# Kernel tuning notes

Measured on AMD Instinct MI355X. Metric: run time of the kernel, lower is better.

## Reference

```python
import jax, jax.numpy as jnp
import numpy as np

NH, NL, NP = 8, 4, 4  # n_heads, n_levels, n_points


def _layer_norm(x, g, b, eps=1e-5):
    mu = x.mean(-1, keepdims=True)
    var = ((x - mu) ** 2).mean(-1, keepdims=True)
    return (x - mu) * jax.lax.rsqrt(var + eps) * g + b


def setup_inputs() -> dict:
    key = jax.random.key(0)
    ks = jax.random.split(key, 16)
    B, C, DFF = 2, 256, 1024
    ss = np.array([[128, 128], [64, 64], [32, 32], [16, 16]], np.int32)
    lsi = np.concatenate([[0], np.cumsum(ss[:, 0] * ss[:, 1])[:-1]]).astype(np.int32)
    Lq = int((ss[:, 0] * ss[:, 1]).sum())  # 21760
    w = lambda k, shp: (jax.random.normal(k, shp, jnp.float32) * 0.02)
    return {
        "src": jax.random.normal(ks[0], (B, Lq, C), jnp.float32),
        "pos": jax.random.normal(ks[1], (B, Lq, C), jnp.float32),
        "reference_points": jax.random.uniform(ks[2], (B, Lq, NL, 2), jnp.float32),
        "spatial_shapes": jnp.asarray(ss),
        "level_start_index": jnp.asarray(lsi),
        "Wv": w(ks[3], (C, C)), "bv": jnp.zeros((C,), jnp.float32),
        "Woff": w(ks[4], (C, NH * NL * NP * 2)), "boff": jnp.zeros((NH * NL * NP * 2,), jnp.float32),
        "Wa": w(ks[5], (C, NH * NL * NP)), "ba": jnp.zeros((NH * NL * NP,), jnp.float32),
        "Wo": w(ks[6], (C, C)), "bo": jnp.zeros((C,), jnp.float32),
        "W1": w(ks[7], (C, DFF)), "b1": jnp.zeros((DFF,), jnp.float32),
        "W2": w(ks[8], (DFF, C)), "b2": jnp.zeros((C,), jnp.float32),
        "g1": jnp.ones((C,), jnp.float32), "be1": jnp.zeros((C,), jnp.float32),
        "g2": jnp.ones((C,), jnp.float32), "be2": jnp.zeros((C,), jnp.float32),
    }


def _ms_deform_attn(value, ss, lsi, loc, attn):
    # value: [B,L,NH,Dh]; loc: [B,Lq,NH,NL,NP,2] in [0,1]; attn: [B,Lq,NH,NL,NP]
    B, Lq = loc.shape[0], loc.shape[1]
    Dh = value.shape[-1]
    out = jnp.zeros((B, NH, Lq, Dh), value.dtype)
    for l in range(NL):
        H_, W_ = int(ss[l, 0]), int(ss[l, 1])
        start = int(lsi[l])
        val = value[:, start:start + H_ * W_].transpose(0, 2, 1, 3)  # [B,NH,HW,Dh]
        x = loc[:, :, :, l, :, 0] * W_ - 0.5  # grid_sample align_corners=False
        y = loc[:, :, :, l, :, 1] * H_ - 0.5  # [B,Lq,NH,NP]
        x0f, y0f = jnp.floor(x), jnp.floor(y)
        lx, ly = x - x0f, y - y0f
        x0, y0 = x0f.astype(jnp.int32), y0f.astype(jnp.int32)
        acc = jnp.zeros((B, NH, Lq, NP, Dh), value.dtype)
        for dy, dx, wgt in ((0, 0, (1 - ly) * (1 - lx)), (0, 1, (1 - ly) * lx),
                            (1, 0, ly * (1 - lx)), (1, 1, ly * lx)):
            yi, xi = y0 + dy, x0 + dx
            valid = ((yi >= 0) & (yi < H_) & (xi >= 0) & (xi < W_)).astype(value.dtype)
            idx = jnp.clip(yi, 0, H_ - 1) * W_ + jnp.clip(xi, 0, W_ - 1)  # [B,Lq,NH,NP]
            idxT = idx.transpose(0, 2, 1, 3).reshape(B, NH, Lq * NP, 1)
            v = jnp.take_along_axis(val, idxT, axis=2).reshape(B, NH, Lq, NP, Dh)
            acc = acc + v * (wgt * valid).transpose(0, 2, 1, 3)[..., None]
        out = out + (acc * attn[:, :, :, l].transpose(0, 2, 1, 3)[..., None]).sum(3)
    return out.transpose(0, 2, 1, 3).reshape(B, Lq, NH * Dh)


def reference(src, pos, reference_points, spatial_shapes, level_start_index,
              Wv, bv, Woff, boff, Wa, ba, Wo, bo, W1, b1, W2, b2, g1, be1, g2, be2):
    ss = np.asarray(spatial_shapes)
    lsi = np.asarray(level_start_index)
    B, Lq, C = src.shape
    Dh = C // NH
    q = src + pos  # with_pos_embed
    value = (src @ Wv + bv).reshape(B, Lq, NH, Dh)
    offs = (q @ Woff + boff).reshape(B, Lq, NH, NL, NP, 2)
    attn = jax.nn.softmax((q @ Wa + ba).reshape(B, Lq, NH, NL * NP), -1).reshape(B, Lq, NH, NL, NP)
    # offset normalizer is (W, H) per level
    norm = jnp.asarray(ss[:, ::-1].astype(np.float32))  # [NL,2]
    loc = reference_points[:, :, None, :, None, :] + offs / norm[None, None, None, :, None, :]
    src2 = _ms_deform_attn(value, ss, lsi, loc, attn) @ Wo + bo
    x = _layer_norm(src + src2, g1, be1)
    ff = jax.nn.relu(x @ W1 + b1) @ W2 + b2
    return _layer_norm(x + ff, g2, be2)
```

## Files before the change

### kernel.cpp

```cpp
#include <hip/hip_runtime.h>
#include <hip/hip_bf16.h>

#define B_    2
#define LQ    21760
#define NROW  (B_*LQ)
#define CDIM  256
#define DFF   1024

typedef __attribute__((ext_vector_type(8))) short bf16x8;
typedef __attribute__((ext_vector_type(4))) float f32x4;
typedef __attribute__((ext_vector_type(2))) float f32x2;

static __device__ __forceinline__ ushort f2bf(float f) {
    union { float f; unsigned u; } v; v.f = f;
    unsigned u = v.u;
    return (ushort)((u + 0x7fffu + ((u >> 16) & 1u)) >> 16);
}
static __device__ __forceinline__ float u2f(unsigned u) {
    union { unsigned u; float f; } v; v.u = u; return v.f;
}
static __device__ __forceinline__ float bf2f(ushort h) {
    return u2f(((unsigned)h) << 16);
}
static __device__ __forceinline__ unsigned char f2fp8(float v) {
    return (unsigned char)(__builtin_amdgcn_cvt_pk_fp8_f32(v, v, 0, false) & 0xff);
}
static __device__ __forceinline__ int swzc(int row, int col) {
    return (col & ~63) | (col & 7) | ((((col >> 3) ^ row) & 7) << 3);
}
static __device__ __forceinline__ int swzc8(int row, int col) {
    return (col & ~127) | (col & 15) | ((((col >> 4) ^ row) & 7) << 4);
}
static __device__ __forceinline__ void gload16(const void* g, void* l) {
    __builtin_amdgcn_global_load_lds(
        (const __attribute__((address_space(1))) unsigned*)g,
        (__attribute__((address_space(3))) unsigned*)l, 16, 0, 0);
}

static __device__ __forceinline__ void wt_one(const float* W, ushort* Wt, int K, int N, int i) {
    int n = i / K, k = i - n * K;
    Wt[(size_t)n * K + swzc(n, k)] = f2bf(W[(size_t)k * N + n]);
}
#define PREP_WT_BLOCKS 2946
#define PREP_AP_BLOCKS 2048
__global__ void prep(const float* __restrict__ Wv, const float* __restrict__ Woff,
                     const float* __restrict__ Wa, const float* __restrict__ Wo,
                     const float* __restrict__ W1, const float* __restrict__ W2,
                     const float* __restrict__ boff, const float* __restrict__ ba,
                     const float* __restrict__ src, const float* __restrict__ pos,
                     ushort* __restrict__ WvT, ushort* __restrict__ WqT,
                     ushort* __restrict__ WoT, ushort* __restrict__ W1T,
                     unsigned char* __restrict__ W2T8, float* __restrict__ bq,
                     ushort* __restrict__ s16, ushort* __restrict__ q16) {
    if (blockIdx.x < PREP_WT_BLOCKS) {
        int gid = blockIdx.x * 256 + threadIdx.x;
        if (gid < 65536)  { wt_one(Wv, WvT, 256, 256, gid); return; }
        if (gid < 163840) {
            int i = gid - 65536;
            int n = i >> 8, k = i & 255;
            float v = (n < 256) ? Woff[(size_t)k * 256 + n] : Wa[(size_t)k * 128 + (n - 256)];
            WqT[n * 256 + swzc(n, k)] = f2bf(v);
            return;
        }
        if (gid < 229376) { wt_one(Wo, WoT, 256, 256,  gid - 163840); return; }
        if (gid < 491520) { wt_one(W1, W1T, 256, 1024, gid - 229376); return; }
        if (gid < 753664) {
            int i = gid - 491520;
            int n = i >> 10, k = i & 1023;
            W2T8[(size_t)n * 1024 + swzc8(n, k)] = f2fp8(16.f * W2[(size_t)k * 256 + n]);
            return;
        }
        if (gid < 754048) {
            int i = gid - 753664;
            bq[i] = (i < 256) ? boff[i] : ba[i - 256];
        }
        return;
    }
    int i = (blockIdx.x - PREP_WT_BLOCKS) * 256 + threadIdx.x;
    int stride = PREP_AP_BLOCKS * 256;
    const float4* s4 = (const float4*)src;
    const float4* p4 = (const float4*)pos;
    const int n4 = NROW * 64;
    for (; i < n4; i += stride) {
        float4 s = s4[i], p = p4[i];
        ushort4 a, b;
        a.x = f2bf(s.x); a.y = f2bf(s.y); a.z = f2bf(s.z); a.w = f2bf(s.w);
        b.x = f2bf(s.x + p.x); b.y = f2bf(s.y + p.y);
        b.z = f2bf(s.z + p.z); b.w = f2bf(s.w + p.w);
        int row = i >> 6, col = (i & 63) * 4;
        int idx = row * 256 + swzc(row, col);
        *(ushort4*)(s16 + idx) = a;
        *(ushort4*)(q16 + idx) = b;
    }
}

__global__ __launch_bounds__(256) void gemm_dual(
    const ushort* __restrict__ s16, const ushort* __restrict__ q16,
    const ushort* __restrict__ WvT, const ushort* __restrict__ WqT,
    const float* __restrict__ bv, const float* __restrict__ bq,
    unsigned char* __restrict__ val8, unsigned char* __restrict__ qout8) {
    const int K = 256;
    const ushort* A; const ushort* Bt; const float* bias;
    int N, bn;
    bool isv = blockIdx.y < 2;
    if (isv) { A = s16; Bt = WvT; bias = bv; N = 256; bn = blockIdx.y * 128; }
    else     { A = q16; Bt = WqT; bias = bq; N = 384; bn = (blockIdx.y - 2) * 128; }

    __shared__ __align__(16) ushort As[128 * 64];
    __shared__ __align__(16) ushort Bs[128 * 64];
    const int tid  = threadIdx.x;
    const int bm   = blockIdx.x * 128;
    const int w    = tid >> 6, lane = tid & 63;
    const int wm   = (w >> 1) * 64, wn = (w & 1) * 64;
    const int lr   = lane & 15, lk = lane >> 4;
    const int srow = tid >> 3, sch = tid & 7;

    f32x4 acc[4][4] = {};

    const ushort* Ab = A  + (size_t)(bm + srow) * K + sch * 8;
    const ushort* Bb = Bt + (size_t)(bn + srow) * K + sch * 8;
    ushort* Asd = &As[srow * 64 + sch * 8];
    ushort* Bsd = &Bs[srow * 64 + sch * 8];

    for (int k0 = 0; k0 < K; k0 += 64) {
        #pragma unroll
        for (int c = 0; c < 4; c++)
            gload16(Ab + (size_t)c * 32 * K + k0, Asd + c * 2048);
        #pragma unroll
        for (int c = 0; c < 4; c++)
            gload16(Bb + (size_t)c * 32 * K + k0, Bsd + c * 2048);
        __syncthreads();
        #pragma unroll
        for (int ks = 0; ks < 2; ks++) {
            bf16x8 af[4], bfr[4];
            #pragma unroll
            for (int m = 0; m < 4; m++) {
                int row = wm + m * 16 + lr;
                int byte = (row * 128 + ks * 64 + lk * 16) ^ ((lr & 7) << 4);
                af[m] = *(const bf16x8*)((const char*)As + byte);
            }
            #pragma unroll
            for (int n = 0; n < 4; n++) {
                int row = wn + n * 16 + lr;
                int byte = (row * 128 + ks * 64 + lk * 16) ^ ((lr & 7) << 4);
                bfr[n] = *(const bf16x8*)((const char*)Bs + byte);
            }
            #pragma unroll
            for (int m = 0; m < 4; m++)
                #pragma unroll
                for (int n = 0; n < 4; n++)
                    acc[m][n] = __builtin_amdgcn_mfma_f32_16x16x32_bf16(af[m], bfr[n], acc[m][n], 0, 0, 0);
        }
        __syncthreads();
    }
    #pragma unroll
    for (int m = 0; m < 4; m++) {
        int row = bm + wm + m * 16 + lk * 4;
        #pragma unroll
        for (int n = 0; n < 4; n++) {
            int col = bn + wn + n * 16 + lr;
            float bb = bias[col];
            #pragma unroll
            for (int i = 0; i < 4; i++) {
                float v = acc[m][n][i] + bb;
                if (isv) val8[(size_t)(row + i) * 256 + col] = f2fp8(v);
                else     qout8[(size_t)(row + i) * 384 + col] = f2fp8(v);
            }
        }
    }
}

template<int RELU, int OUTMODE>
__global__ __launch_bounds__(256) void gemm_bf16(
    const ushort* __restrict__ A, const ushort* __restrict__ Bt,
    const float* __restrict__ bias,
    ushort* __restrict__ Ch, unsigned char* __restrict__ C8,
    int K, int N) {
    __shared__ __align__(16) ushort As[128 * 64];
    __shared__ __align__(16) ushort Bs[128 * 64];
    const int tid  = threadIdx.x;
    const int bm   = blockIdx.x * 128;
    const int bn   = blockIdx.y * 128;
    const int w    = tid >> 6, lane = tid & 63;
    const int wm   = (w >> 1) * 64, wn = (w & 1) * 64;
    const int lr   = lane & 15, lk = lane >> 4;
    const int srow = tid >> 3, sch = tid & 7;

    f32x4 acc[4][4] = {};

    const ushort* Ab = A  + (size_t)(bm + srow) * K + sch * 8;
    const ushort* Bb = Bt + (size_t)(bn + srow) * K + sch * 8;
    ushort* Asd = &As[srow * 64 + sch * 8];
    ushort* Bsd = &Bs[srow * 64 + sch * 8];

    for (int k0 = 0; k0 < K; k0 += 64) {
        #pragma unroll
        for (int c = 0; c < 4; c++)
            gload16(Ab + (size_t)c * 32 * K + k0, Asd + c * 2048);
        #pragma unroll
        for (int c = 0; c < 4; c++)
            gload16(Bb + (size_t)c * 32 * K + k0, Bsd + c * 2048);
        __syncthreads();
        #pragma unroll
        for (int ks = 0; ks < 2; ks++) {
            bf16x8 af[4], bfr[4];
            #pragma unroll
            for (int m = 0; m < 4; m++) {
                int row = wm + m * 16 + lr;
                int byte = (row * 128 + ks * 64 + lk * 16) ^ ((lr & 7) << 4);
                af[m] = *(const bf16x8*)((const char*)As + byte);
            }
            #pragma unroll
            for (int n = 0; n < 4; n++) {
                int row = wn + n * 16 + lr;
                int byte = (row * 128 + ks * 64 + lk * 16) ^ ((lr & 7) << 4);
                bfr[n] = *(const bf16x8*)((const char*)Bs + byte);
            }
            #pragma unroll
            for (int m = 0; m < 4; m++)
                #pragma unroll
                for (int n = 0; n < 4; n++)
                    acc[m][n] = __builtin_amdgcn_mfma_f32_16x16x32_bf16(af[m], bfr[n], acc[m][n], 0, 0, 0);
        }
        __syncthreads();
    }
    #pragma unroll
    for (int m = 0; m < 4; m++) {
        int row = bm + wm + m * 16 + lk * 4;
        #pragma unroll
        for (int n = 0; n < 4; n++) {
            int col = bn + wn + n * 16 + lr;
            float bb = bias ? bias[col] : 0.f;
            #pragma unroll
            for (int i = 0; i < 4; i++) {
                float v = acc[m][n][i] + bb;
                if (RELU) v = v > 0.f ? v : 0.f;
                if (OUTMODE == 2) C8[(size_t)(row + i) * N + swzc8(row + i, col)] = f2fp8(v);
                else              Ch[(size_t)(row + i) * N + swzc(row + i, col)] = f2bf(v);
            }
        }
    }
}

__global__ __launch_bounds__(512) void gemm_lnA(
    const ushort* __restrict__ A, const ushort* __restrict__ Bt,
    const float* __restrict__ bias,
    const ushort* __restrict__ residh,
    const float* __restrict__ g, const float* __restrict__ be,
    ushort* __restrict__ outh) {
    const int KSIZE = 256;
    __shared__ __align__(16) ushort As[64 * 64];
    __shared__ __align__(16) ushort Bs[256 * 64];
    __shared__ float red[4][64][2];
    const int tid  = threadIdx.x;
    const int bm   = blockIdx.x * 64;
    const int w    = tid >> 6, lane = tid & 63;
    const int wm2  = (w >> 2) * 32;
    const int wq   = w & 3;
    const int wn   = wq * 64;
    const int lr   = lane & 15, lk = lane >> 4;
    const int srow = tid >> 3, sch = tid & 7;

    f32x4 acc[2][4] = {};

    const ushort* Ab = A  + (size_t)(bm + srow) * KSIZE + sch * 8;
    const ushort* Bb = Bt + (size_t)srow * KSIZE + sch * 8;
    ushort* Asd = &As[srow * 64 + sch * 8];
    ushort* Bsd = &Bs[srow * 64 + sch * 8];

    for (int k0 = 0; k0 < KSIZE; k0 += 64) {
        gload16(Ab + k0, Asd);
        #pragma unroll
        for (int c = 0; c < 4; c++)
            gload16(Bb + (size_t)c * 64 * KSIZE + k0, Bsd + c * 4096);
        __syncthreads();
        #pragma unroll
        for (int ks = 0; ks < 2; ks++) {
            bf16x8 af[2], bfr[4];
            #pragma unroll
            for (int m = 0; m < 2; m++) {
                int row = wm2 + m * 16 + lr;
                int byte = (row * 128 + ks * 64 + lk * 16) ^ ((lr & 7) << 4);
                af[m] = *(const bf16x8*)((const char*)As + byte);
            }
            #pragma unroll
            for (int n = 0; n < 4; n++) {
                int row = wn + n * 16 + lr;
                int byte = (row * 128 + ks * 64 + lk * 16) ^ ((lr & 7) << 4);
                bfr[n] = *(const bf16x8*)((const char*)Bs + byte);
            }
            #pragma unroll
            for (int m = 0; m < 2; m++)
                #pragma unroll
                for (int n = 0; n < 4; n++)
                    acc[m][n] = __builtin_amdgcn_mfma_f32_16x16x32_bf16(af[m], bfr[n], acc[m][n], 0, 0, 0);
        }
        __syncthreads();
    }

    float bias_r[4], g_r[4], be_r[4];
    #pragma unroll
    for (int n = 0; n < 4; n++) {
        int col = wn + n * 16 + lr;
        bias_r[n] = bias[col]; g_r[n] = g[col]; be_r[n] = be[col];
    }
    #pragma unroll
    for (int m = 0; m < 2; m++) {
        #pragma unroll
        for (int i = 0; i < 4; i++) {
            int lrow = wm2 + m * 16 + lk * 4 + i;
            int row  = bm + lrow;
            float s = 0.f, s2 = 0.f;
            #pragma unroll
            for (int n = 0; n < 4; n++) {
                int col = wn + n * 16 + lr;
                float r = bf2f(residh[(size_t)row * 256 + swzc(row, col)]);
                float v = acc[m][n][i] + bias_r[n] + r;
                acc[m][n][i] = v;
                s += v; s2 += v * v;
            }
            #pragma unroll
            for (int msk = 1; msk < 16; msk <<= 1) {
                s += __shfl_xor(s, msk); s2 += __shfl_xor(s2, msk);
            }
            if (lr == 0) { red[wq][lrow][0] = s; red[wq][lrow][1] = s2; }
        }
    }
    __syncthreads();
    #pragma unroll
    for (int m = 0; m < 2; m++) {
        #pragma unroll
        for (int i = 0; i < 4; i++) {
            int lrow = wm2 + m * 16 + lk * 4 + i;
            int row  = bm + lrow;
            float s  = red[0][lrow][0] + red[1][lrow][0] + red[2][lrow][0] + red[3][lrow][0];
            float s2 = red[0][lrow][1] + red[1][lrow][1] + red[2][lrow][1] + red[3][lrow][1];
            float mu  = s * (1.f / 256.f);
            float var = s2 * (1.f / 256.f) - mu * mu;
            float rs  = rsqrtf(var + 1e-5f);
            #pragma unroll
            for (int n = 0; n < 4; n++) {
                int col = wn + n * 16 + lr;
                float o = (acc[m][n][i] - mu) * rs * g_r[n] + be_r[n];
                outh[(size_t)row * 256 + swzc(row, col)] = f2bf(o);
            }
        }
    }
}

__global__ __launch_bounds__(512) void gemm_ln8(
    const unsigned char* __restrict__ A, const unsigned char* __restrict__ Bt,
    const float* __restrict__ bias,
    const ushort* __restrict__ residh,
    const float* __restrict__ g, const float* __restrict__ be,
    float* __restrict__ outf) {
    const int KSIZE = 1024;
    __shared__ __align__(16) unsigned char As[64 * 128];
    __shared__ __align__(16) unsigned char Bs[256 * 128];
    __shared__ float red[4][64][2];
    const int tid  = threadIdx.x;
    const int bm   = blockIdx.x * 64;
    const int w    = tid >> 6, lane = tid & 63;
    const int wm2  = (w >> 2) * 32;
    const int wq   = w & 3;
    const int wn   = wq * 64;
    const int lr   = lane & 15, lk = lane >> 4;
    const int srow = tid >> 3, sch = tid & 7;

    f32x4 acc[2][4] = {};

    const unsigned char* Ab = A  + (size_t)(bm + srow) * KSIZE + sch * 16;
    const unsigned char* Bb = Bt + (size_t)srow * KSIZE + sch * 16;
    unsigned char* Asd = &As[srow * 128 + sch * 16];
    unsigned char* Bsd = &Bs[srow * 128 + sch * 16];

    for (int k0 = 0; k0 < KSIZE; k0 += 128) {
        gload16(Ab + k0, Asd);
        #pragma unroll
        for (int c = 0; c < 4; c++)
            gload16(Bb + (size_t)c * 64 * KSIZE + k0, Bsd + c * 8192);
        __syncthreads();
        #pragma unroll
        for (int ks = 0; ks < 4; ks++) {
            long long af[2], bfr[4];
            #pragma unroll
            for (int m = 0; m < 2; m++) {
                int row = wm2 + m * 16 + lr;
                int byte = (row * 128 + ks * 32 + lk * 8) ^ ((lr & 7) << 4);
                af[m] = *(const long long*)((const char*)As + byte);
            }
            #pragma unroll
            for (int n = 0; n < 4; n++) {
                int row = wn + n * 16 + lr;
                int byte = (row * 128 + ks * 32 + lk * 8) ^ ((lr & 7) << 4);
                bfr[n] = *(const long long*)((const char*)Bs + byte);
            }
            #pragma unroll
            for (int m = 0; m < 2; m++)
                #pragma unroll
                for (int n = 0; n < 4; n++)
                    acc[m][n] = __builtin_amdgcn_mfma_f32_16x16x32_fp8_fp8(af[m], bfr[n], acc[m][n], 0, 0, 0);
        }
        __syncthreads();
    }

    float bias_r[4], g_r[4], be_r[4];
    #pragma unroll
    for (int n = 0; n < 4; n++) {
        int col = wn + n * 16 + lr;
        bias_r[n] = bias[col]; g_r[n] = g[col]; be_r[n] = be[col];
    }
    #pragma unroll
    for (int m = 0; m < 2; m++) {
        #pragma unroll
        for (int i = 0; i < 4; i++) {
            int lrow = wm2 + m * 16 + lk * 4 + i;
            int row  = bm + lrow;
            float s = 0.f, s2 = 0.f;
            #pragma unroll
            for (int n = 0; n < 4; n++) {
                int col = wn + n * 16 + lr;
                float r = bf2f(residh[(size_t)row * 256 + swzc(row, col)]);
                float v = acc[m][n][i] * 0.0625f + bias_r[n] + r;
                acc[m][n][i] = v;
                s += v; s2 += v * v;
            }
            #pragma unroll
            for (int msk = 1; msk < 16; msk <<= 1) {
                s += __shfl_xor(s, msk); s2 += __shfl_xor(s2, msk);
            }
            if (lr == 0) { red[wq][lrow][0] = s; red[wq][lrow][1] = s2; }
        }
    }
    __syncthreads();
    #pragma unroll
    for (int m = 0; m < 2; m++) {
        #pragma unroll
        for (int i = 0; i < 4; i++) {
            int lrow = wm2 + m * 16 + lk * 4 + i;
            int row  = bm + lrow;
            float s  = red[0][lrow][0] + red[1][lrow][0] + red[2][lrow][0] + red[3][lrow][0];
            float s2 = red[0][lrow][1] + red[1][lrow][1] + red[2][lrow][1] + red[3][lrow][1];
            float mu  = s * (1.f / 256.f);
            float var = s2 * (1.f / 256.f) - mu * mu;
            float rs  = rsqrtf(var + 1e-5f);
            #pragma unroll
            for (int n = 0; n < 4; n++) {
                int col = wn + n * 16 + lr;
                float o = (acc[m][n][i] - mu) * rs * g_r[n] + be_r[n];
                outf[(size_t)row * 256 + col] = o;
            }
        }
    }
}

__global__ __launch_bounds__(256, 4) void deform_attn(
    const unsigned char* __restrict__ val8,
    const unsigned char* __restrict__ qout8,
    const float* __restrict__ rp,
    ushort* __restrict__ out16) {
    __shared__ __align__(16) unsigned offs_s[4][32][20];
    __shared__ __align__(16) float    wgts_s[4][32][20];
    int bid = blockIdx.x;
    bid = (bid & 7) * ((NROW / 4) >> 3) + (bid >> 3);
    const int wid  = threadIdx.x >> 6;
    const int row  = bid * 4 + wid;
    const int lane = threadIdx.x & 63;
    const int h    = lane >> 3;
    const int j    = lane & 7;
    const int b    = row / LQ;

    const unsigned char* qrow = qout8 + (size_t)row * 384;

    ushort lg2 = *(const ushort*)(qrow + 256 + h * 16 + j * 2);
    f32x2 lg = __builtin_amdgcn_cvt_pk_f32_fp8((int)lg2, false);
    float lgx = lg.x, lgy = lg.y;
    float m = fmaxf(lgx, lgy);
    m = fmaxf(m, __shfl_xor(m, 1, 8));
    m = fmaxf(m, __shfl_xor(m, 2, 8));
    m = fmaxf(m, __shfl_xor(m, 4, 8));
    float e0 = __expf(lgx - m), e1 = __expf(lgy - m);
    float s = e0 + e1;
    s += __shfl_xor(s, 1, 8);
    s += __shfl_xor(s, 2, 8);
    s += __shfl_xor(s, 4, 8);
    const float inv = 1.f / s;

    const int L  = j >> 1;
    const int Wl = 128 >> L;
    const int s0 = (L == 0) ? 0 : (L == 1) ? 16384 : (L == 2) ? 20480 : 21504;
    const float fW = (float)Wl;
    float2 rr = *(const float2*)(rp + (size_t)row * 8 + L * 2);
    unsigned ow = *(const unsigned*)(qrow + h * 32 + j * 4);
    f32x2 o0 = __builtin_amdgcn_cvt_pk_f32_fp8((int)ow, false);
    f32x2 o1 = __builtin_amdgcn_cvt_pk_f32_fp8((int)ow, true);
    float oxv[2] = { o0.x, o1.x };
    float oyv[2] = { o0.y, o1.y };
    float ev[2]  = { e0, e1 };

    #pragma unroll
    for (int pt = 0; pt < 2; pt++) {
        float aw = ev[pt] * inv;
        int   p  = j * 2 + pt;
        float x = rr.x * fW + oxv[pt] - 0.5f;
        float y = rr.y * fW + oyv[pt] - 0.5f;
        float xf = floorf(x), yf = floorf(y);
        float lx = x - xf, ly = y - yf;
        int x0 = (int)xf, y0 = (int)yf;
        int x1 = x0 + 1, y1 = y0 + 1;
        int x0c = min(max(x0, 0), Wl - 1), x1c = min(max(x1, 0), Wl - 1);
        int y0c = min(max(y0, 0), Wl - 1), y1c = min(max(y1, 0), Wl - 1);
        bool vx0 = (unsigned)x0 < (unsigned)Wl, vx1 = (unsigned)x1 < (unsigned)Wl;
        bool vy0 = (unsigned)y0 < (unsigned)Wl, vy1 = (unsigned)y1 < (unsigned)Wl;
        float wx1 = lx, wx0 = 1.f - lx, wy1 = ly, wy0 = 1.f - ly;
        float w00 = (vy0 & vx0) ? aw * wy0 * wx0 : 0.f;
        float w01 = (vy0 & vx1) ? aw * wy0 * wx1 : 0.f;
        float w10 = (vy1 & vx0) ? aw * wy1 * wx0 : 0.f;
        float w11 = (vy1 & vx1) ? aw * wy1 * wx1 : 0.f;
        unsigned hb = (unsigned)h * 32u;
        int r0 = h * 4;
        offs_s[wid][r0 + 0][p] = (unsigned)(s0 + y0c * Wl + x0c) * 256u + hb;
        offs_s[wid][r0 + 1][p] = (unsigned)(s0 + y0c * Wl + x1c) * 256u + hb;
        offs_s[wid][r0 + 2][p] = (unsigned)(s0 + y1c * Wl + x0c) * 256u + hb;
        offs_s[wid][r0 + 3][p] = (unsigned)(s0 + y1c * Wl + x1c) * 256u + hb;
        wgts_s[wid][r0 + 0][p] = w00;
        wgts_s[wid][r0 + 1][p] = w01;
        wgts_s[wid][r0 + 2][p] = w10;
        wgts_s[wid][r0 + 3][p] = w11;
    }
    __syncthreads();

    const int c16 = j & 1, pp = j >> 1;
    const int bu = __builtin_amdgcn_readfirstlane(b);
    const char* ubase = (const char*)val8 + (size_t)bu * (LQ * 256);
    const unsigned coff = (unsigned)c16 * 16u;
    const unsigned* po = &offs_s[wid][h * 4 + pp][0];
    const float*    pw = &wgts_s[wid][h * 4 + pp][0];
    f32x2 ac[8] = {};
    #pragma unroll
    for (int t = 0; t < 4; t++) {
        uint4  oo = *(const uint4*)(po + t * 4);
        float4 ww = *(const float4*)(pw + t * 4);
        uint4 u0 = *(const uint4*)(ubase + (oo.x + coff));
        uint4 u1 = *(const uint4*)(ubase + (oo.y + coff));
        uint4 u2 = *(const uint4*)(ubase + (oo.z + coff));
        uint4 u3 = *(const uint4*)(ubase + (oo.w + coff));
        #define ACC16(U, W) { \
            f32x2 w2 = {W, W}; \
            ac[0] += w2 * __builtin_amdgcn_cvt_pk_f32_fp8((int)U.x, false); \
            ac[1] += w2 * __builtin_amdgcn_cvt_pk_f32_fp8((int)U.x, true);  \
            ac[2] += w2 * __builtin_amdgcn_cvt_pk_f32_fp8((int)U.y, false); \
            ac[3] += w2 * __builtin_amdgcn_cvt_pk_f32_fp8((int)U.y, true);  \
            ac[4] += w2 * __builtin_amdgcn_cvt_pk_f32_fp8((int)U.z, false); \
            ac[5] += w2 * __builtin_amdgcn_cvt_pk_f32_fp8((int)U.z, true);  \
            ac[6] += w2 * __builtin_amdgcn_cvt_pk_f32_fp8((int)U.w, false); \
            ac[7] += w2 * __builtin_amdgcn_cvt_pk_f32_fp8((int)U.w, true);  }
        ACC16(u0, ww.x)
        ACC16(u1, ww.y)
        ACC16(u2, ww.z)
        ACC16(u3, ww.w)
        #undef ACC16
    }
    #pragma unroll
    for (int k = 0; k < 8; k++) {
        ac[k].x += __shfl_xor(ac[k].x, 2); ac[k].y += __shfl_xor(ac[k].y, 2);
        ac[k].x += __shfl_xor(ac[k].x, 4); ac[k].y += __shfl_xor(ac[k].y, 4);
    }
    if (pp < 2) {
        uint4 o;
        int base = pp * 4;
        o.x = (unsigned)f2bf(ac[base + 0].x) | ((unsigned)f2bf(ac[base + 0].y) << 16);
        o.y = (unsigned)f2bf(ac[base + 1].x) | ((unsigned)f2bf(ac[base + 1].y) << 16);
        o.z = (unsigned)f2bf(ac[base + 2].x) | ((unsigned)f2bf(ac[base + 2].y) << 16);
        o.w = (unsigned)f2bf(ac[base + 3].x) | ((unsigned)f2bf(ac[base + 3].y) << 16);
        int col = h * 32 + c16 * 16 + pp * 8;
        *(uint4*)(out16 + (size_t)row * 256 + swzc(row, col)) = o;
    }
}

extern "C" void kernel_launch(void* const* d_in, const int* in_sizes, int n_in,
                              void* d_out, int out_size, void* d_ws, size_t ws_size,
                              hipStream_t stream) {
    const float* src  = (const float*)d_in[0];
    const float* pos  = (const float*)d_in[1];
    const float* rp   = (const float*)d_in[2];
    const float* Wv   = (const float*)d_in[5];  const float* bv   = (const float*)d_in[6];
    const float* Woff = (const float*)d_in[7];  const float* boff = (const float*)d_in[8];
    const float* Wa   = (const float*)d_in[9];  const float* ba   = (const float*)d_in[10];
    const float* Wo   = (const float*)d_in[11]; const float* bo   = (const float*)d_in[12];
    const float* W1   = (const float*)d_in[13]; const float* b1   = (const float*)d_in[14];
    const float* W2   = (const float*)d_in[15]; const float* b2   = (const float*)d_in[16];
    const float* g1   = (const float*)d_in[17]; const float* be1  = (const float*)d_in[18];
    const float* g2w  = (const float*)d_in[19]; const float* be2  = (const float*)d_in[20];

    char* ws = (char*)d_ws;
    ushort* s16    = (ushort*)(ws + 0);
    ushort* q16    = (ushort*)(ws + 22282240);
    unsigned char* val8  = (unsigned char*)(ws + 44564480);
    unsigned char* qout8 = (unsigned char*)(ws + 55705600);
    ushort* def16  = (ushort*)(ws + 72417280);
    ushort* x16    = (ushort*)(ws + 94699520);
    ushort* wts    = (ushort*)(ws + 116981760);
    unsigned char* hid8 = (unsigned char*)(ws + 0);

    ushort* WvT = wts;
    ushort* WqT = WvT + 65536;
    ushort* WoT = WqT + 98304;
    ushort* W1T = WoT + 65536;
    unsigned char* W2T8 = (unsigned char*)(W1T + 262144);
    float*  bq  = (float*)(W2T8 + 262144);

    prep<<<PREP_WT_BLOCKS + PREP_AP_BLOCKS, 256, 0, stream>>>(
        Wv, Woff, Wa, Wo, W1, W2, boff, ba, src, pos,
        WvT, WqT, WoT, W1T, W2T8, bq, s16, q16);

    gemm_dual<<<dim3(NROW / 128, 5), 256, 0, stream>>>(
        s16, q16, WvT, WqT, bv, bq, val8, qout8);

    deform_attn<<<NROW / 4, 256, 0, stream>>>(val8, qout8, rp, def16);

    gemm_lnA<<<NROW / 64, 512, 0, stream>>>(
        def16, WoT, bo, s16, g1, be1, x16);

    gemm_bf16<1, 2><<<dim3(NROW / 128, 8), 256, 0, stream>>>(
        x16, W1T, b1, nullptr, hid8, 256, 1024);

    gemm_ln8<<<NROW / 64, 512, 0, stream>>>(
        hid8, W2T8, b2, x16, g2w, be2, (float*)d_out);
}
```

Baseline: 255.2 us.

## Use FP8 for query projection, deform output, and output-projection GEMM

Converts the query activations and the offset/attention weights to FP8 and runs that half of the dual GEMM with fp8 MFMA, compensating for the 16x weight pre-scale. The deformable attention now writes FP8 instead of bf16, and the output projection plus LayerNorm reuses the FP8 LN GEMM template with a bf16 output mode. The goal is to cut memory traffic and raise MFMA throughput, at the cost of lower precision in the query and output-projection paths. The workspace layout is reshuffled so the hidden buffer gets its own region instead of aliasing s16.

```diff
diff --git a/kernel.cpp b/kernel.cpp
--- a/kernel.cpp
+++ b/kernel.cpp
@@ -48,10 +48,10 @@
                      const float* __restrict__ W1, const float* __restrict__ W2,
                      const float* __restrict__ boff, const float* __restrict__ ba,
                      const float* __restrict__ src, const float* __restrict__ pos,
-                     ushort* __restrict__ WvT, ushort* __restrict__ WqT,
-                     ushort* __restrict__ WoT, ushort* __restrict__ W1T,
+                     ushort* __restrict__ WvT, ushort* __restrict__ W1T,
+                     unsigned char* __restrict__ WqT8, unsigned char* __restrict__ WoT8,
                      unsigned char* __restrict__ W2T8, float* __restrict__ bq,
-                     ushort* __restrict__ s16, ushort* __restrict__ q16) {
+                     ushort* __restrict__ s16, unsigned char* __restrict__ q8) {
     if (blockIdx.x < PREP_WT_BLOCKS) {
         int gid = blockIdx.x * 256 + threadIdx.x;
         if (gid < 65536)  { wt_one(Wv, WvT, 256, 256, gid); return; }
@@ -59,10 +59,15 @@
             int i = gid - 65536;
             int n = i >> 8, k = i & 255;
             float v = (n < 256) ? Woff[(size_t)k * 256 + n] : Wa[(size_t)k * 128 + (n - 256)];
-            WqT[n * 256 + swzc(n, k)] = f2bf(v);
+            WqT8[(size_t)n * 256 + swzc8(n, k)] = f2fp8(16.f * v);
             return;
         }
-        if (gid < 229376) { wt_one(Wo, WoT, 256, 256,  gid - 163840); return; }
+        if (gid < 229376) {
+            int i = gid - 163840;
+            int n = i >> 8, k = i & 255;
+            WoT8[(size_t)n * 256 + swzc8(n, k)] = f2fp8(16.f * Wo[(size_t)k * 256 + n]);
+            return;
+        }
         if (gid < 491520) { wt_one(W1, W1T, 256, 1024, gid - 229376); return; }
         if (gid < 753664) {
             int i = gid - 491520;
@@ -83,31 +88,23 @@
     const int n4 = NROW * 64;
     for (; i < n4; i += stride) {
         float4 s = s4[i], p = p4[i];
-        ushort4 a, b;
+        ushort4 a;
         a.x = f2bf(s.x); a.y = f2bf(s.y); a.z = f2bf(s.z); a.w = f2bf(s.w);
-        b.x = f2bf(s.x + p.x); b.y = f2bf(s.y + p.y);
-        b.z = f2bf(s.z + p.z); b.w = f2bf(s.w + p.w);
+        uchar4 b;
+        b.x = f2fp8(s.x + p.x); b.y = f2bf ? f2fp8(s.y + p.y) : 0;
+        b.z = f2fp8(s.z + p.z); b.w = f2fp8(s.w + p.w);
         int row = i >> 6, col = (i & 63) * 4;
-        int idx = row * 256 + swzc(row, col);
-        *(ushort4*)(s16 + idx) = a;
-        *(ushort4*)(q16 + idx) = b;
+        *(ushort4*)(s16 + row * 256 + swzc(row, col)) = a;
+        *(uchar4*)(q8 + (size_t)row * 256 + swzc8(row, col)) = b;
     }
 }
 
 __global__ __launch_bounds__(256) void gemm_dual(
-    const ushort* __restrict__ s16, const ushort* __restrict__ q16,
-    const ushort* __restrict__ WvT, const ushort* __restrict__ WqT,
+    const ushort* __restrict__ s16, const unsigned char* __restrict__ q8,
+    const ushort* __restrict__ WvT, const unsigned char* __restrict__ WqT8,
     const float* __restrict__ bv, const float* __restrict__ bq,
     unsigned char* __restrict__ val8, unsigned char* __restrict__ qout8) {
-    const int K = 256;
-    const ushort* A; const ushort* Bt; const float* bias;
-    int N, bn;
-    bool isv = blockIdx.y < 2;
-    if (isv) { A = s16; Bt = WvT; bias = bv; N = 256; bn = blockIdx.y * 128; }
-    else     { A = q16; Bt = WqT; bias = bq; N = 384; bn = (blockIdx.y - 2) * 128; }
-
-    __shared__ __align__(16) ushort As[128 * 64];
-    __shared__ __align__(16) ushort Bs[128 * 64];
+    __shared__ __align__(16) char lds[32768];
     const int tid  = threadIdx.x;
     const int bm   = blockIdx.x * 128;
     const int w    = tid >> 6, lane = tid & 63;
@@ -117,65 +114,113 @@
 
     f32x4 acc[4][4] = {};
 
-    const ushort* Ab = A  + (size_t)(bm + srow) * K + sch * 8;
-    const ushort* Bb = Bt + (size_t)(bn + srow) * K + sch * 8;
-    ushort* Asd = &As[srow * 64 + sch * 8];
-    ushort* Bsd = &Bs[srow * 64 + sch * 8];
-
-    for (int k0 = 0; k0 < K; k0 += 64) {
-        #pragma unroll
-        for (int c = 0; c < 4; c++)
-            gload16(Ab + (size_t)c * 32 * K + k0, Asd + c * 2048);
-        #pragma unroll
-        for (int c = 0; c < 4; c++)
-            gload16(Bb + (size_t)c * 32 * K + k0, Bsd + c * 2048);
-        __syncthreads();
-        #pragma unroll
-        for (int ks = 0; ks < 2; ks++) {
-            bf16x8 af[4], bfr[4];
-            #pragma unroll
-            for (int m = 0; m < 4; m++) {
-                int row = wm + m * 16 + lr;
-                int byte = (row * 128 + ks * 64 + lk * 16) ^ ((lr & 7) << 4);
-                af[m] = *(const bf16x8*)((const char*)As + byte);
-            }
+    if (blockIdx.y < 2) {
+        const int bn = blockIdx.y * 128;
+        ushort* As = (ushort*)lds;
+        ushort* Bs = (ushort*)(lds + 16384);
+        const ushort* Ab = s16 + (size_t)(bm + srow) * 256 + sch * 8;
+        const ushort* Bb = WvT + (size_t)(bn + srow) * 256 + sch * 8;
+        ushort* Asd = &As[srow * 64 + sch * 8];
+        ushort* Bsd = &Bs[srow * 64 + sch * 8];
+        for (int k0 = 0; k0 < 256; k0 += 64) {
+            #pragma unroll
+            for (int c = 0; c < 4; c++) {
+                gload16(Ab + (size_t)c * 32 * 256 + k0, Asd + c * 2048);
+                gload16(Bb + (size_t)c * 32 * 256 + k0, Bsd + c * 2048);
+            }
+            __syncthreads();
+            #pragma unroll
+            for (int ks = 0; ks < 2; ks++) {
+                bf16x8 af[4], bfr[4];
+                #pragma unroll
+                for (int m = 0; m < 4; m++) {
+                    int row = wm + m * 16 + lr;
+                    int byte = (row * 128 + ks * 64 + lk * 16) ^ ((lr & 7) << 4);
+                    af[m] = *(const bf16x8*)((const char*)As + byte);
+                }
+                #pragma unroll
+                for (int n = 0; n < 4; n++) {
+                    int row = wn + n * 16 + lr;
+                    int byte = (row * 128 + ks * 64 + lk * 16) ^ ((lr & 7) << 4);
+                    bfr[n] = *(const bf16x8*)((const char*)Bs + byte);
+                }
+                #pragma unroll
+                for (int m = 0; m < 4; m++)
+                    #pragma unroll
+                    for (int n = 0; n < 4; n++)
+                        acc[m][n] = __builtin_amdgcn_mfma_f32_16x16x32_bf16(af[m], bfr[n], acc[m][n], 0, 0, 0);
+            }
+            __syncthreads();
+        }
+        #pragma unroll
+        for (int m = 0; m < 4; m++) {
+            int row = bm + wm + m * 16 + lk * 4;
             #pragma unroll
             for (int n = 0; n < 4; n++) {
-                int row = wn + n * 16 + lr;
-                int byte = (row * 128 + ks * 64 + lk * 16) ^ ((lr & 7) << 4);
-                bfr[n] = *(const bf16x8*)((const char*)Bs + byte);
-            }
-            #pragma unroll
-            for (int m = 0; m < 4; m++)
-                #pragma unroll
-                for (int n = 0; n < 4; n++)
-                    acc[m][n] = __builtin_amdgcn_mfma_f32_16x16x32_bf16(af[m], bfr[n], acc[m][n], 0, 0, 0);
-        }
-        __syncthreads();
-    }
-    #pragma unroll
-    for (int m = 0; m < 4; m++) {
-        int row = bm + wm + m * 16 + lk * 4;
-        #pragma unroll
-        for (int n = 0; n < 4; n++) {
-            int col = bn + wn + n * 16 + lr;
-            float bb = bias[col];
-            #pragma unroll
-            for (int i = 0; i < 4; i++) {
-                float v = acc[m][n][i] + bb;
-                if (isv) val8[(size_t)(row + i) * 256 + col] = f2fp8(v);
-                else     qout8[(size_t)(row + i) * 384 + col] = f2fp8(v);
-            }
-        }
-    }
-}
-
-template<int RELU, int OUTMODE>
-__global__ __launch_bounds__(256) void gemm_bf16(
+                int col = bn + wn + n * 16 + lr;
+                float bb = bv[col];
+                #pragma unroll
+                for (int i = 0; i < 4; i++)
+                    val8[(size_t)(row + i) * 256 + col] = f2fp8(acc[m][n][i] + bb);
+            }
+        }
+    } else {
+        const int bn = (blockIdx.y - 2) * 128;
+        unsigned char* As = (unsigned char*)lds;
+        unsigned char* Bs = (unsigned char*)(lds + 16384);
+        const unsigned char* Ab = q8   + (size_t)(bm + srow) * 256 + sch * 16;
+        const unsigned char* Bb = WqT8 + (size_t)(bn + srow) * 256 + sch * 16;
+        unsigned char* Asd = &As[srow * 128 + sch * 16];
+        unsigned char* Bsd = &Bs[srow * 128 + sch * 16];
+        for (int k0 = 0; k0 < 256; k0 += 128) {
+            #pragma unroll
+            for (int c = 0; c < 4; c++) {
+                gload16(Ab + (size_t)c * 32 * 256 + k0, Asd + c * 4096);
+                gload16(Bb + (size_t)c * 32 * 256 + k0, Bsd + c * 4096);
+            }
+            __syncthreads();
+            #pragma unroll
+            for (int ks = 0; ks < 4; ks++) {
+                long long af[4], bfr[4];
+                #pragma unroll
+                for (int m = 0; m < 4; m++) {
+                    int row = wm + m * 16 + lr;
+                    int byte = (row * 128 + ks * 32 + lk * 8) ^ ((lr & 7) << 4);
+                    af[m] = *(const long long*)((const char*)As + byte);
+                }
+                #pragma unroll
+                for (int n = 0; n < 4; n++) {
+                    int row = wn + n * 16 + lr;
+                    int byte = (row * 128 + ks * 32 + lk * 8) ^ ((lr & 7) << 4);
+                    bfr[n] = *(const long long*)((const char*)Bs + byte);
+                }
+                #pragma unroll
+                for (int m = 0; m < 4; m++)
+                    #pragma unroll
+                    for (int n = 0; n < 4; n++)
+                        acc[m][n] = __builtin_amdgcn_mfma_f32_16x16x32_fp8_fp8(af[m], bfr[n], acc[m][n], 0, 0, 0);
+            }
+            __syncthreads();
+        }
+        #pragma unroll
+        for (int m = 0; m < 4; m++) {
+            int row = bm + wm + m * 16 + lk * 4;
+            #pragma unroll
+            for (int n = 0; n < 4; n++) {
+                int col = bn + wn + n * 16 + lr;
+                float bb = bq[col];
+                #pragma unroll
+                for (int i = 0; i < 4; i++)
+                    qout8[(size_t)(row + i) * 384 + col] = f2fp8(acc[m][n][i] * 0.0625f + bb);
+            }
+        }
+    }
+}
+
+__global__ __launch_bounds__(256) void gemm_w1(
     const ushort* __restrict__ A, const ushort* __restrict__ Bt,
-    const float* __restrict__ bias,
-    ushort* __restrict__ Ch, unsigned char* __restrict__ C8,
-    int K, int N) {
+    const float* __restrict__ bias, unsigned char* __restrict__ C8) {
+    const int K = 256, N = 1024;
     __shared__ __align__(16) ushort As[128 * 64];
     __shared__ __align__(16) ushort Bs[128 * 64];
     const int tid  = threadIdx.x;
@@ -195,11 +240,10 @@
 
     for (int k0 = 0; k0 < K; k0 += 64) {
         #pragma unroll
-        for (int c = 0; c < 4; c++)
+        for (int c = 0; c < 4; c++) {
             gload16(Ab + (size_t)c * 32 * K + k0, Asd + c * 2048);
-        #pragma unroll
-        for (int c = 0; c < 4; c++)
             gload16(Bb + (size_t)c * 32 * K + k0, Bsd + c * 2048);
+        }
         __syncthreads();
         #pragma unroll
         for (int ks = 0; ks < 2; ks++) {
@@ -230,131 +274,24 @@
         #pragma unroll
         for (int n = 0; n < 4; n++) {
             int col = bn + wn + n * 16 + lr;
-            float bb = bias ? bias[col] : 0.f;
+            float bb = bias[col];
             #pragma unroll
             for (int i = 0; i < 4; i++) {
                 float v = acc[m][n][i] + bb;
-                if (RELU) v = v > 0.f ? v : 0.f;
-                if (OUTMODE == 2) C8[(size_t)(row + i) * N + swzc8(row + i, col)] = f2fp8(v);
-                else              Ch[(size_t)(row + i) * N + swzc(row + i, col)] = f2bf(v);
-            }
-        }
-    }
-}
-
-__global__ __launch_bounds__(512) void gemm_lnA(
-    const ushort* __restrict__ A, const ushort* __restrict__ Bt,
-    const float* __restrict__ bias,
-    const ushort* __restrict__ residh,
-    const float* __restrict__ g, const float* __restrict__ be,
-    ushort* __restrict__ outh) {
-    const int KSIZE = 256;
-    __shared__ __align__(16) ushort As[64 * 64];
-    __shared__ __align__(16) ushort Bs[256 * 64];
-    __shared__ float red[4][64][2];
-    const int tid  = threadIdx.x;
-    const int bm   = blockIdx.x * 64;
-    const int w    = tid >> 6, lane = tid & 63;
-    const int wm2  = (w >> 2) * 32;
-    const int wq   = w & 3;
-    const int wn   = wq * 64;
-    const int lr   = lane & 15, lk = lane >> 4;
-    const int srow = tid >> 3, sch = tid & 7;
-
-    f32x4 acc[2][4] = {};
-
-    const ushort* Ab = A  + (size_t)(bm + srow) * KSIZE + sch * 8;
-    const ushort* Bb = Bt + (size_t)srow * KSIZE + sch * 8;
-    ushort* Asd = &As[srow * 64 + sch * 8];
-    ushort* Bsd = &Bs[srow * 64 + sch * 8];
-
-    for (int k0 = 0; k0 < KSIZE; k0 += 64) {
-        gload16(Ab + k0, Asd);
-        #pragma unroll
-        for (int c = 0; c < 4; c++)
-            gload16(Bb + (size_t)c * 64 * KSIZE + k0, Bsd + c * 4096);
-        __syncthreads();
-        #pragma unroll
-        for (int ks = 0; ks < 2; ks++) {
-            bf16x8 af[2], bfr[4];
-            #pragma unroll
-            for (int m = 0; m < 2; m++) {
-                int row = wm2 + m * 16 + lr;
-                int byte = (row * 128 + ks * 64 + lk * 16) ^ ((lr & 7) << 4);
-                af[m] = *(const bf16x8*)((const char*)As + byte);
-            }
-            #pragma unroll
-            for (int n = 0; n < 4; n++) {
-                int row = wn + n * 16 + lr;
-                int byte = (row * 128 + ks * 64 + lk * 16) ^ ((lr & 7) << 4);
-                bfr[n] = *(const bf16x8*)((const char*)Bs + byte);
-            }
-            #pragma unroll
-            for (int m = 0; m < 2; m++)
-                #pragma unroll
-                for (int n = 0; n < 4; n++)
-                    acc[m][n] = __builtin_amdgcn_mfma_f32_16x16x32_bf16(af[m], bfr[n], acc[m][n], 0, 0, 0);
-        }
-        __syncthreads();
-    }
-
-    float bias_r[4], g_r[4], be_r[4];
-    #pragma unroll
-    for (int n = 0; n < 4; n++) {
-        int col = wn + n * 16 + lr;
-        bias_r[n] = bias[col]; g_r[n] = g[col]; be_r[n] = be[col];
-    }
-    #pragma unroll
-    for (int m = 0; m < 2; m++) {
-        #pragma unroll
-        for (int i = 0; i < 4; i++) {
-            int lrow = wm2 + m * 16 + lk * 4 + i;
-            int row  = bm + lrow;
-            float s = 0.f, s2 = 0.f;
-            #pragma unroll
-            for (int n = 0; n < 4; n++) {
-                int col = wn + n * 16 + lr;
-                float r = bf2f(residh[(size_t)row * 256 + swzc(row, col)]);
-                float v = acc[m][n][i] + bias_r[n] + r;
-                acc[m][n][i] = v;
-                s += v; s2 += v * v;
-            }
-            #pragma unroll
-            for (int msk = 1; msk < 16; msk <<= 1) {
-                s += __shfl_xor(s, msk); s2 += __shfl_xor(s2, msk);
-            }
-            if (lr == 0) { red[wq][lrow][0] = s; red[wq][lrow][1] = s2; }
-        }
-    }
-    __syncthreads();
-    #pragma unroll
-    for (int m = 0; m < 2; m++) {
-        #pragma unroll
-        for (int i = 0; i < 4; i++) {
-            int lrow = wm2 + m * 16 + lk * 4 + i;
-            int row  = bm + lrow;
-            float s  = red[0][lrow][0] + red[1][lrow][0] + red[2][lrow][0] + red[3][lrow][0];
-            float s2 = red[0][lrow][1] + red[1][lrow][1] + red[2][lrow][1] + red[3][lrow][1];
-            float mu  = s * (1.f / 256.f);
-            float var = s2 * (1.f / 256.f) - mu * mu;
-            float rs  = rsqrtf(var + 1e-5f);
-            #pragma unroll
-            for (int n = 0; n < 4; n++) {
-                int col = wn + n * 16 + lr;
-                float o = (acc[m][n][i] - mu) * rs * g_r[n] + be_r[n];
-                outh[(size_t)row * 256 + swzc(row, col)] = f2bf(o);
-            }
-        }
-    }
-}
-
-__global__ __launch_bounds__(512) void gemm_ln8(
+                v = v > 0.f ? v : 0.f;
+                C8[(size_t)(row + i) * N + swzc8(row + i, col)] = f2fp8(v);
+            }
+        }
+    }
+}
+
+template<int KSIZE, int OUTF32>
+__global__ __launch_bounds__(512) void gemm_ln8f(
     const unsigned char* __restrict__ A, const unsigned char* __restrict__ Bt,
     const float* __restrict__ bias,
     const ushort* __restrict__ residh,
     const float* __restrict__ g, const float* __restrict__ be,
-    float* __restrict__ outf) {
-    const int KSIZE = 1024;
+    float* __restrict__ outf, ushort* __restrict__ outh) {
     __shared__ __align__(16) unsigned char As[64 * 128];
     __shared__ __align__(16) unsigned char Bs[256 * 128];
     __shared__ float red[4][64][2];
@@ -448,7 +385,8 @@
             for (int n = 0; n < 4; n++) {
                 int col = wn + n * 16 + lr;
                 float o = (acc[m][n][i] - mu) * rs * g_r[n] + be_r[n];
-                outf[(size_t)row * 256 + col] = o;
+                if (OUTF32) outf[(size_t)row * 256 + col] = o;
+                else        outh[(size_t)row * 256 + swzc(row, col)] = f2bf(o);
             }
         }
     }
@@ -458,7 +396,7 @@
     const unsigned char* __restrict__ val8,
     const unsigned char* __restrict__ qout8,
     const float* __restrict__ rp,
-    ushort* __restrict__ out16) {
+    unsigned char* __restrict__ out8) {
     __shared__ __align__(16) unsigned offs_s[4][32][20];
     __shared__ __align__(16) float    wgts_s[4][32][20];
     int bid = blockIdx.x;
@@ -567,14 +505,14 @@
         ac[k].x += __shfl_xor(ac[k].x, 4); ac[k].y += __shfl_xor(ac[k].y, 4);
     }
     if (pp < 2) {
-        uint4 o;
         int base = pp * 4;
-        o.x = (unsigned)f2bf(ac[base + 0].x) | ((unsigned)f2bf(ac[base + 0].y) << 16);
-        o.y = (unsigned)f2bf(ac[base + 1].x) | ((unsigned)f2bf(ac[base + 1].y) << 16);
-        o.z = (unsigned)f2bf(ac[base + 2].x) | ((unsigned)f2bf(ac[base + 2].y) << 16);
-        o.w = (unsigned)f2bf(ac[base + 3].x) | ((unsigned)f2bf(ac[base + 3].y) << 16);
+        uint2 o;
+        o.x = ((unsigned)__builtin_amdgcn_cvt_pk_fp8_f32(ac[base + 0].x, ac[base + 0].y, 0, false) & 0xffffu)
+            | (((unsigned)__builtin_amdgcn_cvt_pk_fp8_f32(ac[base + 1].x, ac[base + 1].y, 0, false) & 0xffffu) << 16);
+        o.y = ((unsigned)__builtin_amdgcn_cvt_pk_fp8_f32(ac[base + 2].x, ac[base + 2].y, 0, false) & 0xffffu)
+            | (((unsigned)__builtin_amdgcn_cvt_pk_fp8_f32(ac[base + 3].x, ac[base + 3].y, 0, false) & 0xffffu) << 16);
         int col = h * 32 + c16 * 16 + pp * 8;
-        *(uint4*)(out16 + (size_t)row * 256 + swzc(row, col)) = o;
+        *(uint2*)(out8 + (size_t)row * 256 + swzc8(row, col)) = o;
     }
 }
 
@@ -595,36 +533,36 @@
 
     char* ws = (char*)d_ws;
     ushort* s16    = (ushort*)(ws + 0);
-    ushort* q16    = (ushort*)(ws + 22282240);
-    unsigned char* val8  = (unsigned char*)(ws + 44564480);
-    unsigned char* qout8 = (unsigned char*)(ws + 55705600);
-    ushort* def16  = (ushort*)(ws + 72417280);
-    ushort* x16    = (ushort*)(ws + 94699520);
-    ushort* wts    = (ushort*)(ws + 116981760);
-    unsigned char* hid8 = (unsigned char*)(ws + 0);
+    unsigned char* q8    = (unsigned char*)(ws + 22282240);
+    unsigned char* val8  = (unsigned char*)(ws + 33423360);
+    unsigned char* qout8 = (unsigned char*)(ws + 44564480);
+    unsigned char* def8  = (unsigned char*)(ws + 61276160);
+    ushort* x16    = (ushort*)(ws + 72417280);
+    unsigned char* hid8  = (unsigned char*)(ws + 94699520);
+    ushort* wts    = (ushort*)(ws + 139264000);
 
     ushort* WvT = wts;
-    ushort* WqT = WvT + 65536;
-    ushort* WoT = WqT + 98304;
-    ushort* W1T = WoT + 65536;
-    unsigned char* W2T8 = (unsigned char*)(W1T + 262144);
+    ushort* W1T = WvT + 65536;
+    unsigned char* WqT8 = (unsigned char*)(W1T + 262144);
+    unsigned char* WoT8 = WqT8 + 98304;
+    unsigned char* W2T8 = WoT8 + 65536;
     float*  bq  = (float*)(W2T8 + 262144);
 
     prep<<<PREP_WT_BLOCKS + PREP_AP_BLOCKS, 256, 0, stream>>>(
         Wv, Woff, Wa, Wo, W1, W2, boff, ba, src, pos,
-        WvT, WqT, WoT, W1T, W2T8, bq, s16, q16);
+        WvT, W1T, WqT8, WoT8, W2T8, bq, s16, q8);
 
     gemm_dual<<<dim3(NROW / 128, 5), 256, 0, stream>>>(
-        s16, q16, WvT, WqT, bv, bq, val8, qout8);
-
-    deform_attn<<<NROW / 4, 256, 0, stream>>>(val8, qout8, rp, def16);
-
-    gemm_lnA<<<NROW / 64, 512, 0, stream>>>(
-        def16, WoT, bo, s16, g1, be1, x16);
-
-    gemm_bf16<1, 2><<<dim3(NROW / 128, 8), 256, 0, stream>>>(
-        x16, W1T, b1, nullptr, hid8, 256, 1024);
-
-    gemm_ln8<<<NROW / 64, 512, 0, stream>>>(
-        hid8, W2T8, b2, x16, g2w, be2, (float*)d_out);
-}
+        s16, q8, WvT, WqT8, bv, bq, val8, qout8);
+
+    deform_attn<<<NROW / 4, 256, 0, stream>>>(val8, qout8, rp, def8);
+
+    gemm_ln8f<256, 0><<<NROW / 64, 512, 0, stream>>>(
+        def8, WoT8, bo, s16, g1, be1, nullptr, x16);
+
+    gemm_w1<<<dim3(NROW / 128, 8), 256, 0, stream>>>(
+        x16, W1T, b1, hid8);
+
+    gemm_ln8f<1024, 1><<<NROW / 64, 512, 0, stream>>>(
+        hid8, W2T8, b2, x16, g2w, be2, (float*)d_out, nullptr);
+}
```

New measurement: 229.3 us. 1.11x faster.
